# Kernel tuning notes

Hardware: AMD Instinct MI355X
Metric: run time of the kernel (lower is better)

The kernel has to match this reference:

```python
import jax, jax.numpy as jnp
import numpy as np

N, E = 100000, 1600000
IN_C, H, C = 256, 4, 64
NEG_SLOPE = 0.2


def setup_inputs() -> dict:
    key = jax.random.key(0)
    k1, k2, k3, k4, k5 = jax.random.split(key, 5)
    x = jax.random.normal(k1, (N, IN_C), dtype=jnp.float32)
    edge_index = jax.random.randint(k2, (2, E), 0, N, dtype=jnp.int64)
    # GATConv params: lin weight [IN_C, H*C], attention vectors [H, C], bias [C] (concat=False)
    W = jax.random.normal(k3, (IN_C, H * C), dtype=jnp.float32) / np.sqrt(IN_C)
    att_src = jax.random.normal(k4, (H, C), dtype=jnp.float32) / np.sqrt(C)
    att_dst = jax.random.normal(k5, (H, C), dtype=jnp.float32) / np.sqrt(C)
    bias = jnp.zeros((C,), dtype=jnp.float32)
    return {"x": x, "edge_index": edge_index, "W": W,
            "att_src": att_src, "att_dst": att_dst, "bias": bias}


def reference(x, edge_index, W, att_src, att_dst, bias):
    n = x.shape[0]
    # GATConv adds self-loops by default
    loops = jnp.arange(n, dtype=edge_index.dtype)
    src = jnp.concatenate([edge_index[0], loops])  # message source j
    dst = jnp.concatenate([edge_index[1], loops])  # message target i

    h = (x @ W).reshape(n, H, C)                       # [N,H,C]
    a_src = jnp.einsum('nhc,hc->nh', h, att_src)       # [N,H]
    a_dst = jnp.einsum('nhc,hc->nh', h, att_dst)       # [N,H]

    e = jax.nn.leaky_relu(a_src[src] + a_dst[dst], NEG_SLOPE)  # [E+N,H]
    m = jax.ops.segment_max(e, dst, num_segments=n)            # per-target max
    e = jnp.exp(e - m[dst])
    denom = jax.ops.segment_sum(e, dst, num_segments=n)
    alpha = e / (denom[dst] + 1e-16)                           # softmax over incoming edges

    out = jax.ops.segment_sum(alpha[:, :, None] * h[src], dst, num_segments=n)  # [N,H,C]
    return out.mean(axis=1) + bias  # concat=False -> mean over heads, [N,C]
```

## Files before the change

kernel.cpp:

```cpp
#include <hip/hip_runtime.h>

#define N_NODES 100000
#define N_EDGES 1600000
#define TOT (N_EDGES + N_NODES)
#define IN_CH 256
#define NHEAD 4
#define CH 64
#define HC 256
#define NEG_SLOPE 0.2f
#define NGEMM ((N_NODES + 63) / 64)
#define DEG_BLOCKS 391
#define NBLK1 ((N_NODES + 1023) / 1024)

typedef _Float16 half8 __attribute__((ext_vector_type(8)));
typedef _Float16 h2v __attribute__((ext_vector_type(2)));
typedef float f32x4 __attribute__((ext_vector_type(4)));
typedef unsigned short ushort_t;
typedef unsigned int uint_t;

static __device__ __forceinline__ ushort_t f2h(float f) {
  _Float16 h = (_Float16)f;
  return __builtin_bit_cast(ushort_t, h);
}

static __device__ __forceinline__ void gload_lds16(const char* g, char* l) {
  __builtin_amdgcn_global_load_lds(
      (const __attribute__((address_space(1))) unsigned int*)g,
      (__attribute__((address_space(3))) unsigned int*)l, 16, 0, 0);
}

__global__ __launch_bounds__(256) void conv_w(const float* __restrict__ W,
                                              uint4* __restrict__ Wt_arr,
                                              int* __restrict__ deg) {
  int id = blockIdx.x * 256 + threadIdx.x;
  int lane = id & 63;
  int n = (id >> 6) & 15;
  int ks = id >> 10;
  int col = n * 16 + (lane & 15);
  int kbase = ks * 32 + (lane >> 4) * 8;
  ushort_t h[8];
#pragma unroll
  for (int j = 0; j < 8; ++j) h[j] = f2h(W[(size_t)(kbase + j) * HC + col]);
  uint4 u;
  u.x = (uint_t)h[0] | ((uint_t)h[1] << 16);
  u.y = (uint_t)h[2] | ((uint_t)h[3] << 16);
  u.z = (uint_t)h[4] | ((uint_t)h[5] << 16);
  u.w = (uint_t)h[6] | ((uint_t)h[7] << 16);
  Wt_arr[id] = u;
  for (int i = id; i < N_NODES / 4; i += 8192)
    reinterpret_cast<int4*>(deg)[i] = make_int4(0, 0, 0, 0);
}

__global__ __launch_bounds__(256) void gemm_mfma(const float* __restrict__ X,
                                                 const uint4* __restrict__ Wt_arr,
                                                 const float* __restrict__ att_src,
                                                 const float* __restrict__ att_dst,
                                                 uint2* __restrict__ Hmp,
                                                 float* __restrict__ as_out,
                                                 float* __restrict__ ad_out,
                                                 const int* __restrict__ edst,
                                                 int* __restrict__ deg, int M) {
  const int tid = threadIdx.x;

  if (blockIdx.x < DEG_BLOCKS) {
#pragma unroll
    for (int i = 0; i < 4; ++i) {
      int t = (blockIdx.x * 4 + i) * 256 + tid;
      if (t < N_EDGES / 4) {
        int4 d4 = reinterpret_cast<const int4*>(edst)[t];
        atomicAdd(&deg[d4.x], 1);
        atomicAdd(&deg[d4.y], 1);
        atomicAdd(&deg[d4.z], 1);
        atomicAdd(&deg[d4.w], 1);
      }
    }
    return;
  }

  __shared__ uint4 Bs[3][1024];
  __shared__ __align__(16) float As[3][2048];
  const int lane = tid & 63;
  const int wid = tid >> 6;
  const int l16 = lane & 15;
  const int lhi = lane >> 4;
  const int row0 = (blockIdx.x - DEG_BLOCKS) * 64;

  const int arow = tid >> 3;
  const int aslot = tid & 7;
  int ga0 = row0 + arow;       if (ga0 >= M) ga0 = M - 1;
  int ga1 = row0 + arow + 32;  if (ga1 >= M) ga1 = M - 1;
  const int sslot = aslot ^ (arow & 7);
  const char* asrc0 = (const char*)X + (size_t)ga0 * 1024 + (sslot << 4);
  const char* asrc1 = (const char*)X + (size_t)ga1 * 1024 + (sslot << 4);

  const char* __restrict__ wsrc = (const char*)Wt_arr;

  const int frow = wid * 16 + l16;
  const int sw = frow & 7;
  const int fo0 = frow * 32 + (((2 * lhi + 0) ^ sw) << 2);
  const int fo1 = frow * 32 + (((2 * lhi + 1) ^ sw) << 2);

  auto ISSUE = [&](int kk, int b) {
    char* ad = (char*)&As[b][0] + tid * 16;
    gload_lds16(asrc0 + kk * 128, ad);
    gload_lds16(asrc1 + kk * 128, ad + 4096);
    char* bd = (char*)&Bs[b][0] + tid * 16;
    const char* s = wsrc + kk * 16384 + tid * 16;
    gload_lds16(s,         bd);
    gload_lds16(s + 4096,  bd + 4096);
    gload_lds16(s + 8192,  bd + 8192);
    gload_lds16(s + 12288, bd + 12288);
  };

  ISSUE(0, 0);
  ISSUE(1, 1);

  f32x4 acc[16] = {};

#pragma unroll
  for (int ks = 0; ks < 8; ++ks) {
    __builtin_amdgcn_s_barrier();
    if (ks < 6) ISSUE(ks + 2, (ks + 2) % 3);
    if (ks < 6)       asm volatile("s_waitcnt vmcnt(12)" ::: "memory");
    else if (ks == 6) asm volatile("s_waitcnt vmcnt(6)" ::: "memory");
    else              asm volatile("s_waitcnt vmcnt(0)" ::: "memory");

    const float* Ab = &As[ks % 3][0];
    float4 f0 = *reinterpret_cast<const float4*>(Ab + fo0);
    float4 f1 = *reinterpret_cast<const float4*>(Ab + fo1);
    uint4 ua;
    ua.x = __builtin_bit_cast(uint_t, __builtin_amdgcn_cvt_pkrtz(f0.x, f0.y));
    ua.y = __builtin_bit_cast(uint_t, __builtin_amdgcn_cvt_pkrtz(f0.z, f0.w));
    ua.z = __builtin_bit_cast(uint_t, __builtin_amdgcn_cvt_pkrtz(f1.x, f1.y));
    ua.w = __builtin_bit_cast(uint_t, __builtin_amdgcn_cvt_pkrtz(f1.z, f1.w));
    half8 a = __builtin_bit_cast(half8, ua);

    const char* bbase = (const char*)&Bs[ks % 3][0];
#pragma unroll
    for (int n = 0; n < 16; ++n) {
      half8 b = *reinterpret_cast<const half8*>(bbase + n * 1024 + lane * 16);
      acc[n] = __builtin_amdgcn_mfma_f32_16x16x32_f16(a, b, acc[n], 0, 0, 0);
    }
  }

  float attS[16], attD[16];
#pragma unroll
  for (int n = 0; n < 16; ++n) {
    attS[n] = att_src[n * 16 + l16];
    attD[n] = att_dst[n * 16 + l16];
  }

#pragma unroll
  for (int r = 0; r < 4; ++r) {
    int grow = row0 + wid * 16 + lhi * 4 + r;
    if (grow < M) {
#pragma unroll
      for (int n2 = 0; n2 < 4; ++n2) {
        uint_t pk01 = __builtin_bit_cast(uint_t,
            __builtin_amdgcn_cvt_pkrtz(acc[n2][r], acc[n2 + 4][r]));
        uint_t pk23 = __builtin_bit_cast(uint_t,
            __builtin_amdgcn_cvt_pkrtz(acc[n2 + 8][r], acc[n2 + 12][r]));
        Hmp[(size_t)grow * 64 + n2 * 16 + l16] = make_uint2(pk01, pk23);
      }
      float sv[4] = {0.f, 0.f, 0.f, 0.f}, dv[4] = {0.f, 0.f, 0.f, 0.f};
#pragma unroll
      for (int h = 0; h < 4; ++h)
#pragma unroll
        for (int j = 0; j < 4; ++j) {
          sv[h] += acc[h * 4 + j][r] * attS[h * 4 + j];
          dv[h] += acc[h * 4 + j][r] * attD[h * 4 + j];
        }
#pragma unroll
      for (int off = 1; off < 16; off <<= 1)
#pragma unroll
        for (int h = 0; h < 4; ++h) {
          sv[h] += __shfl_xor(sv[h], off, 16);
          dv[h] += __shfl_xor(dv[h], off, 16);
        }
      if (l16 == 0) {
#pragma unroll
        for (int h = 0; h < 4; ++h) {
          as_out[(size_t)grow * 4 + h] = sv[h];
          ad_out[(size_t)grow * 4 + h] = dv[h];
        }
      }
    }
  }
}

__global__ __launch_bounds__(256) void scan1(const int* __restrict__ deg,
                                             int* __restrict__ rp,
                                             int* __restrict__ bsum) {
  __shared__ int sh[256];
  int t = threadIdx.x;
  int base = blockIdx.x * 1024 + t * 4;
  int v[4];
#pragma unroll
  for (int i = 0; i < 4; ++i) v[i] = (base + i < N_NODES) ? (deg[base + i] + 1) : 0;
  int tsum = v[0] + v[1] + v[2] + v[3];
  sh[t] = tsum;
  __syncthreads();
  for (int off = 1; off < 256; off <<= 1) {
    int x = (t >= off) ? sh[t - off] : 0;
    __syncthreads();
    sh[t] += x;
    __syncthreads();
  }
  if (t == 255) bsum[blockIdx.x] = sh[255];
  int run = sh[t] - tsum;
#pragma unroll
  for (int i = 0; i < 4; ++i) {
    if (base + i < N_NODES) rp[base + i] = run;
    run += v[i];
  }
}

__global__ __launch_bounds__(256) void scan23(int* __restrict__ rp,
                                              const int* __restrict__ bsum,
                                              int* __restrict__ cursor) {
  __shared__ int inc[128];
  int t = threadIdx.x;
  if (t < 128) inc[t] = (t < NBLK1) ? bsum[t] : 0;
  __syncthreads();
  for (int off = 1; off < 128; off <<= 1) {
    int x = 0;
    if (t < 128 && t >= off) x = inc[t - off];
    __syncthreads();
    if (t < 128) inc[t] += x;
    __syncthreads();
  }
  int idx = blockIdx.x * 256 + t;
  if (idx < N_NODES) {
    int c = idx >> 10;
    int boff = inc[c] - bsum[c];
    int v = rp[idx] + boff;
    rp[idx] = v;
    cursor[idx] = v;
  }
  if (idx == 0) rp[N_NODES] = TOT;
}

__global__ __launch_bounds__(256) void scatter_edges(const int* __restrict__ esrc,
                                                     const int* __restrict__ edst,
                                                     const float* __restrict__ as_buf,
                                                     const float* __restrict__ ad_buf,
                                                     int* __restrict__ cursor,
                                                     uint4* __restrict__ erec) {
  int e = blockIdx.x * 256 + threadIdx.x;
  if (e >= TOT) return;
  int s, d;
  if (e < N_EDGES) { s = esrc[e]; d = edst[e]; }
  else { s = e - N_EDGES; d = s; }
  int p = atomicAdd(&cursor[d], 1);
  float4 a1 = *reinterpret_cast<const float4*>(as_buf + (size_t)s * NHEAD);
  float4 a2 = *reinterpret_cast<const float4*>(ad_buf + (size_t)d * NHEAD);
  float e0 = a1.x + a2.x; e0 = e0 > 0.f ? e0 : NEG_SLOPE * e0;
  float e1 = a1.y + a2.y; e1 = e1 > 0.f ? e1 : NEG_SLOPE * e1;
  float e2 = a1.z + a2.z; e2 = e2 > 0.f ? e2 : NEG_SLOPE * e2;
  float e3 = a1.w + a2.w; e3 = e3 > 0.f ? e3 : NEG_SLOPE * e3;
  float w0 = __expf(e0 - 4.f), w1 = __expf(e1 - 4.f);
  float w2 = __expf(e2 - 4.f), w3 = __expf(e3 - 4.f);
  uint_t pk01 = __builtin_bit_cast(uint_t, __builtin_amdgcn_cvt_pkrtz(w0, w1));
  uint_t pk23 = __builtin_bit_cast(uint_t, __builtin_amdgcn_cvt_pkrtz(w2, w3));
  erec[p] = make_uint4((uint_t)s, pk01, pk23, 0u);
}

static __device__ __forceinline__ void accum_edge(uint4 cur, uint4 hv, bool act,
                                                  float* acc, float* den) {
  uint_t w01u = act ? cur.y : 0u;
  uint_t w23u = act ? cur.z : 0u;
  h2v w01 = __builtin_bit_cast(h2v, w01u);
  h2v w23 = __builtin_bit_cast(h2v, w23u);
  h2v ha = __builtin_bit_cast(h2v, hv.x);
  h2v hb = __builtin_bit_cast(h2v, hv.y);
  h2v hc = __builtin_bit_cast(h2v, hv.z);
  h2v hd = __builtin_bit_cast(h2v, hv.w);
  acc[0] += (float)w01.x * (float)ha.x;
  acc[1] += (float)w01.y * (float)ha.y;
  acc[2] += (float)w23.x * (float)hb.x;
  acc[3] += (float)w23.y * (float)hb.y;
  acc[4] += (float)w01.x * (float)hc.x;
  acc[5] += (float)w01.y * (float)hc.y;
  acc[6] += (float)w23.x * (float)hd.x;
  acc[7] += (float)w23.y * (float)hd.y;
  den[0] += (float)w01.x;
  den[1] += (float)w01.y;
  den[2] += (float)w23.x;
  den[3] += (float)w23.y;
}

__global__ __launch_bounds__(256) void aggregate(const int* __restrict__ rp,
                                                 const uint4* __restrict__ erec,
                                                 const uint2* __restrict__ Hp,
                                                 const float* __restrict__ bias,
                                                 float* __restrict__ out) {
  int n = blockIdx.x * 4 + (threadIdx.x >> 6);
  int lane = threadIdx.x & 63;
  if (n >= N_NODES) return;
  const int half = lane >> 5;
  const uint_t off_lane = (uint_t)(lane & 31) << 4;
  const char* __restrict__ Hb = (const char*)Hp;

  int beg = rp[n], end = rp[n + 1];
  const int last = end - 1;

  float acc[8] = {};
  float den[4] = {};

  int i0 = beg + half;     if (i0 > last) i0 = last;
  int i1 = beg + 2 + half; if (i1 > last) i1 = last;
  int i2 = beg + 4 + half; if (i2 > last) i2 = last;
  int i3 = beg + 6 + half; if (i3 > last) i3 = last;
  uint4 r0 = erec[i0], r1 = erec[i1], r2 = erec[i2], r3 = erec[i3];

  for (int j = beg; j < end; j += 8) {
    uint4 c0 = r0, c1 = r1, c2 = r2, c3 = r3;
    i0 = j + 8 + half;  if (i0 > last) i0 = last;
    i1 = j + 10 + half; if (i1 > last) i1 = last;
    i2 = j + 12 + half; if (i2 > last) i2 = last;
    i3 = j + 14 + half; if (i3 > last) i3 = last;
    r0 = erec[i0]; r1 = erec[i1]; r2 = erec[i2]; r3 = erec[i3];

    uint4 h0 = *reinterpret_cast<const uint4*>(Hb + ((c0.x << 9) | off_lane));
    uint4 h1 = *reinterpret_cast<const uint4*>(Hb + ((c1.x << 9) | off_lane));
    uint4 h2 = *reinterpret_cast<const uint4*>(Hb + ((c2.x << 9) | off_lane));
    uint4 h3 = *reinterpret_cast<const uint4*>(Hb + ((c3.x << 9) | off_lane));

    accum_edge(c0, h0, (j + half) < end, acc, den);
    accum_edge(c1, h1, (j + 2 + half) < end, acc, den);
    accum_edge(c2, h2, (j + 4 + half) < end, acc, den);
    accum_edge(c3, h3, (j + 6 + half) < end, acc, den);
  }

#pragma unroll
  for (int k = 0; k < 8; ++k) acc[k] += __shfl_xor(acc[k], 32, 64);
#pragma unroll
  for (int k = 0; k < 4; ++k) den[k] += __shfl_xor(den[k], 32, 64);

  if (lane < 32) {
    float i0v = 1.f / (den[0] + 1e-30f);
    float i1v = 1.f / (den[1] + 1e-30f);
    float i2v = 1.f / (den[2] + 1e-30f);
    float i3v = 1.f / (den[3] + 1e-30f);
    float2 b2 = *reinterpret_cast<const float2*>(bias + 2 * lane);
    float rA = 0.25f * (acc[0] * i0v + acc[1] * i1v + acc[2] * i2v + acc[3] * i3v) + b2.x;
    float rB = 0.25f * (acc[4] * i0v + acc[5] * i1v + acc[6] * i2v + acc[7] * i3v) + b2.y;
    *reinterpret_cast<float2*>(out + (size_t)n * CH + 2 * lane) = make_float2(rA, rB);
  }
}

extern "C" void kernel_launch(void* const* d_in, const int* in_sizes, int n_in,
                              void* d_out, int out_size, void* d_ws, size_t ws_size,
                              hipStream_t stream) {
  const float* x       = (const float*)d_in[0];
  const int*   eidx    = (const int*)d_in[1];
  const float* W       = (const float*)d_in[2];
  const float* att_src = (const float*)d_in[3];
  const float* att_dst = (const float*)d_in[4];
  const float* bias    = (const float*)d_in[5];
  float* out = (float*)d_out;

  uint2* Hmp    = (uint2*)d_ws;
  uint4* erec   = (uint4*)(Hmp + (size_t)N_NODES * 64);
  float* as_buf = (float*)(erec + (size_t)TOT + 16);
  float* ad_buf = as_buf + (size_t)N_NODES * NHEAD;
  uint4* Wt_arr = (uint4*)(ad_buf + (size_t)N_NODES * NHEAD);
  int*   deg    = (int*)(Wt_arr + 8192);
  int*   rp     = deg + N_NODES;
  int*   bsum   = rp + N_NODES + 1;

  const int* esrc = eidx;
  const int* edst = eidx + N_EDGES;

  conv_w<<<32, 256, 0, stream>>>(W, Wt_arr, deg);

  dim3 ggrid(DEG_BLOCKS + NGEMM);
  gemm_mfma<<<ggrid, 256, 0, stream>>>(x, Wt_arr, att_src, att_dst, Hmp, as_buf, ad_buf,
                                       edst, deg, N_NODES);

  scan1<<<NBLK1, 256, 0, stream>>>(deg, rp, bsum);
  scan23<<<(N_NODES + 255) / 256, 256, 0, stream>>>(rp, bsum, deg );
  scatter_edges<<<(TOT + 255) / 256, 256, 0, stream>>>(esrc, edst, as_buf, ad_buf,
                                                       deg , erec);

  aggregate<<<(N_NODES + 3) / 4, 256, 0, stream>>>(rp, erec, Hmp, bias, out);
}
```

Baseline: 309.6 us.

## Precompute W·att vectors for attention logits and co-schedule GEMM with edge scatter

```diff
diff --git a/kernel.cpp b/kernel.cpp
--- a/kernel.cpp
+++ b/kernel.cpp
@@ -10,6 +10,8 @@
 #define NEG_SLOPE 0.2f
 #define NGEMM ((N_NODES + 63) / 64)
 #define DEG_BLOCKS 391
+#define DOTS_BLOCKS ((N_NODES + 3) / 4)
+#define SCT_BLOCKS ((TOT + 255) / 256)
 #define NBLK1 ((N_NODES + 1023) / 1024)
 
 typedef _Float16 half8 __attribute__((ext_vector_type(8)));
@@ -30,8 +32,30 @@
 }
 
 __global__ __launch_bounds__(256) void conv_w(const float* __restrict__ W,
+                                              const float* __restrict__ att_src,
+                                              const float* __restrict__ att_dst,
                                               uint4* __restrict__ Wt_arr,
+                                              float4* __restrict__ Was4,
+                                              float4* __restrict__ Wad4,
                                               int* __restrict__ deg) {
+  if (blockIdx.x == 32) {
+    int k = threadIdx.x;
+    float s[4] = {}, d[4] = {};
+#pragma unroll
+    for (int h = 0; h < 4; ++h) {
+      const float4* wr = reinterpret_cast<const float4*>(W + (size_t)k * HC + h * 64);
+      const float4* asr = reinterpret_cast<const float4*>(att_src + h * 64);
+      const float4* adr = reinterpret_cast<const float4*>(att_dst + h * 64);
+      for (int c4 = 0; c4 < 16; ++c4) {
+        float4 w = wr[c4], a = asr[c4], b = adr[c4];
+        s[h] += w.x * a.x + w.y * a.y + w.z * a.z + w.w * a.w;
+        d[h] += w.x * b.x + w.y * b.y + w.z * b.z + w.w * b.w;
+      }
+    }
+    Was4[k] = make_float4(s[0], s[1], s[2], s[3]);
+    Wad4[k] = make_float4(d[0], d[1], d[2], d[3]);
+    return;
+  }
   int id = blockIdx.x * 256 + threadIdx.x;
   int lane = id & 63;
   int n = (id >> 6) & 15;
@@ -51,17 +75,14 @@
     reinterpret_cast<int4*>(deg)[i] = make_int4(0, 0, 0, 0);
 }
 
-__global__ __launch_bounds__(256) void gemm_mfma(const float* __restrict__ X,
-                                                 const uint4* __restrict__ Wt_arr,
-                                                 const float* __restrict__ att_src,
-                                                 const float* __restrict__ att_dst,
-                                                 uint2* __restrict__ Hmp,
-                                                 float* __restrict__ as_out,
-                                                 float* __restrict__ ad_out,
-                                                 const int* __restrict__ edst,
-                                                 int* __restrict__ deg, int M) {
+__global__ __launch_bounds__(256) void deg_dots(const int* __restrict__ edst,
+                                                int* __restrict__ deg,
+                                                const float* __restrict__ X,
+                                                const float4* __restrict__ Was4,
+                                                const float4* __restrict__ Wad4,
+                                                float* __restrict__ as_buf,
+                                                float* __restrict__ ad_buf) {
   const int tid = threadIdx.x;
-
   if (blockIdx.x < DEG_BLOCKS) {
 #pragma unroll
     for (int i = 0; i < 4; ++i) {
@@ -76,115 +97,31 @@
     }
     return;
   }
-
-  __shared__ uint4 Bs[3][1024];
-  __shared__ __align__(16) float As[3][2048];
-  const int lane = tid & 63;
-  const int wid = tid >> 6;
-  const int l16 = lane & 15;
-  const int lhi = lane >> 4;
-  const int row0 = (blockIdx.x - DEG_BLOCKS) * 64;
-
-  const int arow = tid >> 3;
-  const int aslot = tid & 7;
-  int ga0 = row0 + arow;       if (ga0 >= M) ga0 = M - 1;
-  int ga1 = row0 + arow + 32;  if (ga1 >= M) ga1 = M - 1;
-  const int sslot = aslot ^ (arow & 7);
-  const char* asrc0 = (const char*)X + (size_t)ga0 * 1024 + (sslot << 4);
-  const char* asrc1 = (const char*)X + (size_t)ga1 * 1024 + (sslot << 4);
-
-  const char* __restrict__ wsrc = (const char*)Wt_arr;
-
-  const int frow = wid * 16 + l16;
-  const int sw = frow & 7;
-  const int fo0 = frow * 32 + (((2 * lhi + 0) ^ sw) << 2);
-  const int fo1 = frow * 32 + (((2 * lhi + 1) ^ sw) << 2);
-
-  auto ISSUE = [&](int kk, int b) {
-    char* ad = (char*)&As[b][0] + tid * 16;
-    gload_lds16(asrc0 + kk * 128, ad);
-    gload_lds16(asrc1 + kk * 128, ad + 4096);
-    char* bd = (char*)&Bs[b][0] + tid * 16;
-    const char* s = wsrc + kk * 16384 + tid * 16;
-    gload_lds16(s,         bd);
-    gload_lds16(s + 4096,  bd + 4096);
-    gload_lds16(s + 8192,  bd + 8192);
-    gload_lds16(s + 12288, bd + 12288);
-  };
-
-  ISSUE(0, 0);
-  ISSUE(1, 1);
-
-  f32x4 acc[16] = {};
-
-#pragma unroll
-  for (int ks = 0; ks < 8; ++ks) {
-    __builtin_amdgcn_s_barrier();
-    if (ks < 6) ISSUE(ks + 2, (ks + 2) % 3);
-    if (ks < 6)       asm volatile("s_waitcnt vmcnt(12)" ::: "memory");
-    else if (ks == 6) asm volatile("s_waitcnt vmcnt(6)" ::: "memory");
-    else              asm volatile("s_waitcnt vmcnt(0)" ::: "memory");
-
-    const float* Ab = &As[ks % 3][0];
-    float4 f0 = *reinterpret_cast<const float4*>(Ab + fo0);
-    float4 f1 = *reinterpret_cast<const float4*>(Ab + fo1);
-    uint4 ua;
-    ua.x = __builtin_bit_cast(uint_t, __builtin_amdgcn_cvt_pkrtz(f0.x, f0.y));
-    ua.y = __builtin_bit_cast(uint_t, __builtin_amdgcn_cvt_pkrtz(f0.z, f0.w));
-    ua.z = __builtin_bit_cast(uint_t, __builtin_amdgcn_cvt_pkrtz(f1.x, f1.y));
-    ua.w = __builtin_bit_cast(uint_t, __builtin_amdgcn_cvt_pkrtz(f1.z, f1.w));
-    half8 a = __builtin_bit_cast(half8, ua);
-
-    const char* bbase = (const char*)&Bs[ks % 3][0];
-#pragma unroll
-    for (int n = 0; n < 16; ++n) {
-      half8 b = *reinterpret_cast<const half8*>(bbase + n * 1024 + lane * 16);
-      acc[n] = __builtin_amdgcn_mfma_f32_16x16x32_f16(a, b, acc[n], 0, 0, 0);
+  int n = (blockIdx.x - DEG_BLOCKS) * 4 + (tid >> 6);
+  int lane = tid & 63;
+  if (n >= N_NODES) return;
+  float4 xv = reinterpret_cast<const float4*>(X)[(size_t)n * 64 + lane];
+  const float4* ws = Was4 + lane * 4;
+  const float4* wd = Wad4 + lane * 4;
+  float s[4] = {}, d[4] = {};
+  float xj[4] = {xv.x, xv.y, xv.z, xv.w};
+#pragma unroll
+  for (int j = 0; j < 4; ++j) {
+    float4 a = ws[j], b = wd[j];
+    s[0] += xj[j] * a.x; s[1] += xj[j] * a.y; s[2] += xj[j] * a.z; s[3] += xj[j] * a.w;
+    d[0] += xj[j] * b.x; d[1] += xj[j] * b.y; d[2] += xj[j] * b.z; d[3] += xj[j] * b.w;
+  }
+#pragma unroll
+  for (int off = 32; off > 0; off >>= 1) {
+#pragma unroll
+    for (int h = 0; h < 4; ++h) {
+      s[h] += __shfl_xor(s[h], off, 64);
+      d[h] += __shfl_xor(d[h], off, 64);
     }
   }
-
-  float attS[16], attD[16];
-#pragma unroll
-  for (int n = 0; n < 16; ++n) {
-    attS[n] = att_src[n * 16 + l16];
-    attD[n] = att_dst[n * 16 + l16];
-  }
-
-#pragma unroll
-  for (int r = 0; r < 4; ++r) {
-    int grow = row0 + wid * 16 + lhi * 4 + r;
-    if (grow < M) {
-#pragma unroll
-      for (int n2 = 0; n2 < 4; ++n2) {
-        uint_t pk01 = __builtin_bit_cast(uint_t,
-            __builtin_amdgcn_cvt_pkrtz(acc[n2][r], acc[n2 + 4][r]));
-        uint_t pk23 = __builtin_bit_cast(uint_t,
-            __builtin_amdgcn_cvt_pkrtz(acc[n2 + 8][r], acc[n2 + 12][r]));
-        Hmp[(size_t)grow * 64 + n2 * 16 + l16] = make_uint2(pk01, pk23);
-      }
-      float sv[4] = {0.f, 0.f, 0.f, 0.f}, dv[4] = {0.f, 0.f, 0.f, 0.f};
-#pragma unroll
-      for (int h = 0; h < 4; ++h)
-#pragma unroll
-        for (int j = 0; j < 4; ++j) {
-          sv[h] += acc[h * 4 + j][r] * attS[h * 4 + j];
-          dv[h] += acc[h * 4 + j][r] * attD[h * 4 + j];
-        }
-#pragma unroll
-      for (int off = 1; off < 16; off <<= 1)
-#pragma unroll
-        for (int h = 0; h < 4; ++h) {
-          sv[h] += __shfl_xor(sv[h], off, 16);
-          dv[h] += __shfl_xor(dv[h], off, 16);
-        }
-      if (l16 == 0) {
-#pragma unroll
-        for (int h = 0; h < 4; ++h) {
-          as_out[(size_t)grow * 4 + h] = sv[h];
-          ad_out[(size_t)grow * 4 + h] = dv[h];
-        }
-      }
-    }
+  if (lane == 0) {
+    *reinterpret_cast<float4*>(as_buf + (size_t)n * 4) = make_float4(s[0], s[1], s[2], s[3]);
+    *reinterpret_cast<float4*>(ad_buf + (size_t)n * 4) = make_float4(d[0], d[1], d[2], d[3]);
   }
 }
 
@@ -240,29 +177,118 @@
   if (idx == 0) rp[N_NODES] = TOT;
 }
 
-__global__ __launch_bounds__(256) void scatter_edges(const int* __restrict__ esrc,
-                                                     const int* __restrict__ edst,
-                                                     const float* __restrict__ as_buf,
-                                                     const float* __restrict__ ad_buf,
-                                                     int* __restrict__ cursor,
-                                                     uint4* __restrict__ erec) {
-  int e = blockIdx.x * 256 + threadIdx.x;
-  if (e >= TOT) return;
-  int s, d;
-  if (e < N_EDGES) { s = esrc[e]; d = edst[e]; }
-  else { s = e - N_EDGES; d = s; }
-  int p = atomicAdd(&cursor[d], 1);
-  float4 a1 = *reinterpret_cast<const float4*>(as_buf + (size_t)s * NHEAD);
-  float4 a2 = *reinterpret_cast<const float4*>(ad_buf + (size_t)d * NHEAD);
-  float e0 = a1.x + a2.x; e0 = e0 > 0.f ? e0 : NEG_SLOPE * e0;
-  float e1 = a1.y + a2.y; e1 = e1 > 0.f ? e1 : NEG_SLOPE * e1;
-  float e2 = a1.z + a2.z; e2 = e2 > 0.f ? e2 : NEG_SLOPE * e2;
-  float e3 = a1.w + a2.w; e3 = e3 > 0.f ? e3 : NEG_SLOPE * e3;
-  float w0 = __expf(e0 - 4.f), w1 = __expf(e1 - 4.f);
-  float w2 = __expf(e2 - 4.f), w3 = __expf(e3 - 4.f);
-  uint_t pk01 = __builtin_bit_cast(uint_t, __builtin_amdgcn_cvt_pkrtz(w0, w1));
-  uint_t pk23 = __builtin_bit_cast(uint_t, __builtin_amdgcn_cvt_pkrtz(w2, w3));
-  erec[p] = make_uint4((uint_t)s, pk01, pk23, 0u);
+__global__ __launch_bounds__(256) void scatter_gemm(const int* __restrict__ esrc,
+                                                    const int* __restrict__ edst,
+                                                    const float* __restrict__ as_buf,
+                                                    const float* __restrict__ ad_buf,
+                                                    int* __restrict__ cursor,
+                                                    uint4* __restrict__ erec,
+                                                    const float* __restrict__ X,
+                                                    const uint4* __restrict__ Wt_arr,
+                                                    uint2* __restrict__ Hmp, int M) {
+  const int tid = threadIdx.x;
+
+  if (blockIdx.x < SCT_BLOCKS) {
+    int e = blockIdx.x * 256 + tid;
+    if (e >= TOT) return;
+    int s, d;
+    if (e < N_EDGES) { s = esrc[e]; d = edst[e]; }
+    else { s = e - N_EDGES; d = s; }
+    int p = atomicAdd(&cursor[d], 1);
+    float4 a1 = *reinterpret_cast<const float4*>(as_buf + (size_t)s * NHEAD);
+    float4 a2 = *reinterpret_cast<const float4*>(ad_buf + (size_t)d * NHEAD);
+    float e0 = a1.x + a2.x; e0 = e0 > 0.f ? e0 : NEG_SLOPE * e0;
+    float e1 = a1.y + a2.y; e1 = e1 > 0.f ? e1 : NEG_SLOPE * e1;
+    float e2 = a1.z + a2.z; e2 = e2 > 0.f ? e2 : NEG_SLOPE * e2;
+    float e3 = a1.w + a2.w; e3 = e3 > 0.f ? e3 : NEG_SLOPE * e3;
+    float w0 = __expf(e0 - 4.f), w1 = __expf(e1 - 4.f);
+    float w2 = __expf(e2 - 4.f), w3 = __expf(e3 - 4.f);
+    uint_t pk01 = __builtin_bit_cast(uint_t, __builtin_amdgcn_cvt_pkrtz(w0, w1));
+    uint_t pk23 = __builtin_bit_cast(uint_t, __builtin_amdgcn_cvt_pkrtz(w2, w3));
+    erec[p] = make_uint4((uint_t)s, pk01, pk23, 0u);
+    return;
+  }
+
+  __shared__ uint4 Bs[3][1024];
+  __shared__ __align__(16) float As[3][2048];
+  const int lane = tid & 63;
+  const int wid = tid >> 6;
+  const int l16 = lane & 15;
+  const int lhi = lane >> 4;
+  const int row0 = (blockIdx.x - SCT_BLOCKS) * 64;
+
+  const int arow = tid >> 3;
+  const int aslot = tid & 7;
+  int ga0 = row0 + arow;       if (ga0 >= M) ga0 = M - 1;
+  int ga1 = row0 + arow + 32;  if (ga1 >= M) ga1 = M - 1;
+  const int sslot = aslot ^ (arow & 7);
+  const char* asrc0 = (const char*)X + (size_t)ga0 * 1024 + (sslot << 4);
+  const char* asrc1 = (const char*)X + (size_t)ga1 * 1024 + (sslot << 4);
+
+  const char* __restrict__ wsrc = (const char*)Wt_arr;
+
+  const int frow = wid * 16 + l16;
+  const int sw = frow & 7;
+  const int fo0 = frow * 32 + (((2 * lhi + 0) ^ sw) << 2);
+  const int fo1 = frow * 32 + (((2 * lhi + 1) ^ sw) << 2);
+
+  auto ISSUE = [&](int kk, int b) {
+    char* ad = (char*)&As[b][0] + tid * 16;
+    gload_lds16(asrc0 + kk * 128, ad);
+    gload_lds16(asrc1 + kk * 128, ad + 4096);
+    char* bd = (char*)&Bs[b][0] + tid * 16;
+    const char* s = wsrc + kk * 16384 + tid * 16;
+    gload_lds16(s,         bd);
+    gload_lds16(s + 4096,  bd + 4096);
+    gload_lds16(s + 8192,  bd + 8192);
+    gload_lds16(s + 12288, bd + 12288);
+  };
+
+  ISSUE(0, 0);
+  ISSUE(1, 1);
+
+  f32x4 acc[16] = {};
+
+#pragma unroll
+  for (int ks = 0; ks < 8; ++ks) {
+    __builtin_amdgcn_s_barrier();
+    if (ks < 6) ISSUE(ks + 2, (ks + 2) % 3);
+    if (ks < 6)       asm volatile("s_waitcnt vmcnt(12)" ::: "memory");
+    else if (ks == 6) asm volatile("s_waitcnt vmcnt(6)" ::: "memory");
+    else              asm volatile("s_waitcnt vmcnt(0)" ::: "memory");
+
+    const float* Ab = &As[ks % 3][0];
+    float4 f0 = *reinterpret_cast<const float4*>(Ab + fo0);
+    float4 f1 = *reinterpret_cast<const float4*>(Ab + fo1);
+    uint4 ua;
+    ua.x = __builtin_bit_cast(uint_t, __builtin_amdgcn_cvt_pkrtz(f0.x, f0.y));
+    ua.y = __builtin_bit_cast(uint_t, __builtin_amdgcn_cvt_pkrtz(f0.z, f0.w));
+    ua.z = __builtin_bit_cast(uint_t, __builtin_amdgcn_cvt_pkrtz(f1.x, f1.y));
+    ua.w = __builtin_bit_cast(uint_t, __builtin_amdgcn_cvt_pkrtz(f1.z, f1.w));
+    half8 a = __builtin_bit_cast(half8, ua);
+
+    const char* bbase = (const char*)&Bs[ks % 3][0];
+#pragma unroll
+    for (int n = 0; n < 16; ++n) {
+      half8 b = *reinterpret_cast<const half8*>(bbase + n * 1024 + lane * 16);
+      acc[n] = __builtin_amdgcn_mfma_f32_16x16x32_f16(a, b, acc[n], 0, 0, 0);
+    }
+  }
+
+#pragma unroll
+  for (int r = 0; r < 4; ++r) {
+    int grow = row0 + wid * 16 + lhi * 4 + r;
+    if (grow < M) {
+#pragma unroll
+      for (int n2 = 0; n2 < 4; ++n2) {
+        uint_t pk01 = __builtin_bit_cast(uint_t,
+            __builtin_amdgcn_cvt_pkrtz(acc[n2][r], acc[n2 + 4][r]));
+        uint_t pk23 = __builtin_bit_cast(uint_t,
+            __builtin_amdgcn_cvt_pkrtz(acc[n2 + 8][r], acc[n2 + 12][r]));
+        Hmp[(size_t)grow * 64 + n2 * 16 + l16] = make_uint2(pk01, pk23);
+      }
+    }
+  }
 }
 
 static __device__ __forceinline__ void accum_edge(uint4 cur, uint4 hv, bool act,
@@ -360,28 +386,31 @@
   const float* bias    = (const float*)d_in[5];
   float* out = (float*)d_out;
 
-  uint2* Hmp    = (uint2*)d_ws;
-  uint4* erec   = (uint4*)(Hmp + (size_t)N_NODES * 64);
-  float* as_buf = (float*)(erec + (size_t)TOT + 16);
-  float* ad_buf = as_buf + (size_t)N_NODES * NHEAD;
-  uint4* Wt_arr = (uint4*)(ad_buf + (size_t)N_NODES * NHEAD);
-  int*   deg    = (int*)(Wt_arr + 8192);
-  int*   rp     = deg + N_NODES;
-  int*   bsum   = rp + N_NODES + 1;
+  uint2*  Hmp    = (uint2*)d_ws;
+  uint4*  erec   = (uint4*)(Hmp + (size_t)N_NODES * 64);
+  float*  as_buf = (float*)(erec + (size_t)TOT + 16);
+  float*  ad_buf = as_buf + (size_t)N_NODES * NHEAD;
+  uint4*  Wt_arr = (uint4*)(ad_buf + (size_t)N_NODES * NHEAD);
+  float4* Was4   = (float4*)(Wt_arr + 8192);
+  float4* Wad4   = Was4 + 256;
+  int*    deg    = (int*)(Wad4 + 256);
+  int*    rp     = deg + N_NODES;
+  int*    bsum   = rp + N_NODES + 1;
 
   const int* esrc = eidx;
   const int* edst = eidx + N_EDGES;
 
-  conv_w<<<32, 256, 0, stream>>>(W, Wt_arr, deg);
-
-  dim3 ggrid(DEG_BLOCKS + NGEMM);
-  gemm_mfma<<<ggrid, 256, 0, stream>>>(x, Wt_arr, att_src, att_dst, Hmp, as_buf, ad_buf,
-                                       edst, deg, N_NODES);
+  conv_w<<<33, 256, 0, stream>>>(W, att_src, att_dst, Wt_arr, Was4, Wad4, deg);
+
+  deg_dots<<<DEG_BLOCKS + DOTS_BLOCKS, 256, 0, stream>>>(edst, deg, x, Was4, Wad4,
+                                                         as_buf, ad_buf);
 
   scan1<<<NBLK1, 256, 0, stream>>>(deg, rp, bsum);
   scan23<<<(N_NODES + 255) / 256, 256, 0, stream>>>(rp, bsum, deg );
-  scatter_edges<<<(TOT + 255) / 256, 256, 0, stream>>>(esrc, edst, as_buf, ad_buf,
-                                                       deg , erec);
+
+  scatter_gemm<<<SCT_BLOCKS + NGEMM, 256, 0, stream>>>(esrc, edst, as_buf, ad_buf,
+                                                       deg , erec, x, Wt_arr,
+                                                       Hmp, N_NODES);
 
   aggregate<<<(N_NODES + 3) / 4, 256, 0, stream>>>(rp, erec, Hmp, bias, out);
 }
```

Result: slower. 354.2 us (+14.4%).
